# Performance work log

Hardware: AMD Instinct MI355X
Metric: run time of the kernel (lower is better)

The kernel has to match this reference:

```python
import jax, jax.numpy as jnp
import numpy as np

EMBED = 1024
HEADS = 16
HEAD_DIM = EMBED // HEADS
B, S = 4, 2048


def setup_inputs() -> dict:
    key = jax.random.key(0)
    ks = jax.random.split(key, 12)
    scale = 1.0 / np.sqrt(EMBED)
    inp = {
        'query': jax.random.normal(ks[0], (B, S, EMBED), jnp.float32),
        'key_in': jax.random.normal(ks[1], (B, S, EMBED), jnp.float32),
        'value': jax.random.normal(ks[2], (B, S, EMBED), jnp.float32),
        'mask': jnp.tril(jnp.ones((S, S), jnp.int32))[None, None],  # causal [1,1,S,S]
        'Wq': jax.random.normal(ks[3], (EMBED, EMBED), jnp.float32) * scale,
        'bq': jnp.zeros((EMBED,), jnp.float32),
        'Wk': jax.random.normal(ks[4], (EMBED, EMBED), jnp.float32) * scale,
        'bk': jnp.zeros((EMBED,), jnp.float32),
        'Wv': jax.random.normal(ks[5], (EMBED, EMBED), jnp.float32) * scale,
        'bv': jnp.zeros((EMBED,), jnp.float32),
        'Wo': jax.random.normal(ks[6], (EMBED, EMBED), jnp.float32) * scale,
        'bo': jnp.zeros((EMBED,), jnp.float32),
    }
    return inp


def reference(query, key_in, value, mask, Wq, bq, Wk, bk, Wv, bv, Wo, bo):
    b = query.shape[0]
    # projections (torch Linear: x @ W.T + b)
    Q = query @ Wq.T + bq
    K = key_in @ Wk.T + bk
    V = value @ Wv.T + bv
    # [B, H, S, Dh]
    Q = Q.reshape(b, -1, HEADS, HEAD_DIM).transpose(0, 2, 1, 3)
    K = K.reshape(b, -1, HEADS, HEAD_DIM).transpose(0, 2, 1, 3)
    V = V.reshape(b, -1, HEADS, HEAD_DIM).transpose(0, 2, 1, 3)
    scores = jnp.einsum('bhqd,bhkd->bhqk', Q, K) / np.sqrt(HEAD_DIM)
    scores = jnp.where(mask == 0, jnp.float32(-1e20), scores)
    probs = jax.nn.softmax(scores, axis=-1)  # dropout p=0 (eval)
    attn = jnp.einsum('bhqk,bhkd->bhqd', probs, V)
    attn = attn.transpose(0, 2, 1, 3).reshape(b, -1, EMBED)
    return attn @ Wo.T + bo
```

## Files before the change

kernel.cpp:

```cpp
#include <hip/hip_runtime.h>

typedef unsigned short u16;
typedef __bf16 bf16x8 __attribute__((ext_vector_type(8)));
typedef float f32x4 __attribute__((ext_vector_type(4)));

#define EMBED   1024
#define HEADS   16
#define HEAD_DIM 64
#define BATCH   4
#define SEQ     2048
#define MROWS   (BATCH * SEQ)

__device__ __forceinline__ u16 f2bf(float f) {
  union { __bf16 h; u16 u; } c;
  c.h = (__bf16)f;
  return c.u;
}

__device__ __forceinline__ bf16x8 cvt8(const float* p) {
  const float4 a = *(const float4*)p;
  const float4 b = *(const float4*)(p + 4);
  bf16x8 r;
  r[0] = (__bf16)a.x; r[1] = (__bf16)a.y; r[2] = (__bf16)a.z; r[3] = (__bf16)a.w;
  r[4] = (__bf16)b.x; r[5] = (__bf16)b.y; r[6] = (__bf16)b.z; r[7] = (__bf16)b.w;
  return r;
}

__device__ __forceinline__ void gload16(const u16* g, u16* lds) {
  __builtin_amdgcn_global_load_lds(
      (const __attribute__((address_space(1))) void*)g,
      (__attribute__((address_space(3))) void*)lds, 16, 0, 0);
}

__global__ __launch_bounds__(256) void cvt_bf16(
    const float* __restrict__ src, u16* __restrict__ dst, int n8)
{
  const int i = blockIdx.x * 256 + threadIdx.x;
  if (i < n8) *(bf16x8*)(dst + (size_t)i * 8) = cvt8(src + (size_t)i * 8);
}

__global__ __launch_bounds__(256) void cvt_a(
    const float* k,  u16* dk,  const float* v,  u16* dv,
    const float* wq, u16* dwq, const float* wk, u16* dwk,
    const float* wv, u16* dwv, int n8t, int n8w)
{
  int i = blockIdx.x * 256 + threadIdx.x;
  if (i < n8t) { *(bf16x8*)(dk + (size_t)i * 8) = cvt8(k + (size_t)i * 8); return; }
  i -= n8t;
  if (i < n8t) { *(bf16x8*)(dv + (size_t)i * 8) = cvt8(v + (size_t)i * 8); return; }
  i -= n8t;
  if (i < n8w) { *(bf16x8*)(dwq + (size_t)i * 8) = cvt8(wq + (size_t)i * 8); return; }
  i -= n8w;
  if (i < n8w) { *(bf16x8*)(dwk + (size_t)i * 8) = cvt8(wk + (size_t)i * 8); return; }
  i -= n8w;
  if (i < n8w) { *(bf16x8*)(dwv + (size_t)i * 8) = cvt8(wv + (size_t)i * 8); }
}

__device__ __forceinline__ void swz_block(int& m0, int& n0) {
  int bid = blockIdx.y * 8 + blockIdx.x;
  bid = (bid & 7) * 64 + (bid >> 3);
  m0 = (bid >> 3) * 128;
  n0 = (bid & 7) * 128;
}

#define GT_BK  64
#define GT_NT  (EMBED / GT_BK)
#define GT_BUF (128 * GT_BK * 2)

__global__ __launch_bounds__(256, 2) void gemm10(
    const u16* __restrict__ Aa, const u16* __restrict__ Ab,
    const u16* __restrict__ Wa, const u16* __restrict__ Wb,
    const float* __restrict__ biasa, const float* __restrict__ biasb,
    void* __restrict__ Ca, void* __restrict__ Cb, int fmode)
{
  __shared__ __align__(16) u16 smem[2 * GT_BUF];

  const int z = blockIdx.z;
  const u16* A      = z ? Ab : Aa;
  const u16* Bw     = z ? Wb : Wa;
  const float* bias = z ? biasb : biasa;
  void* C = z ? Cb : Ca;
  const int mode = z ? 1 : fmode;

  const int t    = threadIdx.x;
  const int lane = t & 63;
  const int wave = t >> 6;
  const int quad = lane >> 4;
  const int lr   = lane & 15;
  const int wr   = (wave >> 1) * 64;
  const int wc   = (wave & 1) * 64;
  int m0, n0;
  swz_block(m0, n0);

  const int sr = lane >> 3;
  const int sc = ((lane & 7) ^ sr) * 8;

  auto stage = [&](int b, int tt) {
    const int kb = tt * GT_BK;
    u16* s = smem + b * GT_BUF;
#pragma unroll
    for (int c8 = 0; c8 < 4; ++c8) {
      const int g = wave * 32 + c8 * 8;
      gload16(&A [(size_t)(m0 + g + sr) * EMBED + kb + sc], s + g * GT_BK);
      gload16(&Bw[(size_t)(n0 + g + sr) * EMBED + kb + sc], s + 128 * GT_BK + g * GT_BK);
    }
  };

  auto fragA = [&](int b, int mi, int ks) -> bf16x8 {
    const int row = wr + mi * 16 + lr;
    return *(const bf16x8*)(smem + b * GT_BUF + row * GT_BK
                            + (((ks * 4 + quad) ^ (row & 7)) << 3));
  };
  auto fragB = [&](int b, int ni, int ks) -> bf16x8 {
    const int row = wc + ni * 16 + lr;
    return *(const bf16x8*)(smem + b * GT_BUF + 128 * GT_BK + row * GT_BK
                            + (((ks * 4 + quad) ^ (row & 7)) << 3));
  };

  f32x4 acc[4][4] = {};

  stage(0, 0);
  asm volatile("s_waitcnt vmcnt(0)" ::: "memory");
  __builtin_amdgcn_s_barrier();
  __builtin_amdgcn_sched_barrier(0);

#pragma unroll 1
  for (int tt = 0; tt < GT_NT; ++tt) {
    const int cb = tt & 1;
    if (tt + 1 < GT_NT) stage(cb ^ 1, tt + 1);
#pragma unroll
    for (int ks = 0; ks < 2; ++ks) {
      bf16x8 af[4], bfr[4];
#pragma unroll
      for (int i = 0; i < 4; ++i) af[i]  = fragA(cb, i, ks);
#pragma unroll
      for (int i = 0; i < 4; ++i) bfr[i] = fragB(cb, i, ks);
      __builtin_amdgcn_s_setprio(1);
#pragma unroll
      for (int mi = 0; mi < 4; ++mi)
#pragma unroll
        for (int ni = 0; ni < 4; ++ni)
          acc[mi][ni] = __builtin_amdgcn_mfma_f32_16x16x32_bf16(af[mi], bfr[ni], acc[mi][ni], 0, 0, 0);
      __builtin_amdgcn_s_setprio(0);
    }
    asm volatile("s_waitcnt vmcnt(0)" ::: "memory");
    __builtin_amdgcn_s_barrier();
    __builtin_amdgcn_sched_barrier(0);
  }

  if (mode == 1) {
    u16* Vt = (u16*)C;
#pragma unroll
    for (int mi = 0; mi < 4; ++mi)
#pragma unroll
      for (int ni = 0; ni < 4; ++ni) {
        const int col = n0 + wc + ni * 16 + lr;
        const int hh = col >> 6, dd = col & 63;
        const float bv = bias[col];
        const int row0 = m0 + wr + mi * 16 + quad * 4;
        const int bb = row0 >> 11, s0 = row0 & 2047;
        u16 pk[4];
#pragma unroll
        for (int r = 0; r < 4; ++r) pk[r] = f2bf(acc[mi][ni][r] + bv);
        *(ushort4*)&Vt[((size_t)((bb * 16 + hh) * 64 + dd)) * SEQ + s0] = *(ushort4*)pk;
      }
  } else if (mode == 2) {
    float* Cf = (float*)C;
#pragma unroll
    for (int mi = 0; mi < 4; ++mi)
#pragma unroll
      for (int ni = 0; ni < 4; ++ni) {
        const int col = n0 + wc + ni * 16 + lr;
        const float bv = bias[col];
#pragma unroll
        for (int r = 0; r < 4; ++r) {
          const int row = m0 + wr + mi * 16 + quad * 4 + r;
          Cf[(size_t)row * EMBED + col] = acc[mi][ni][r] + bv;
        }
      }
  } else {
    u16* Cu = (u16*)C;
#pragma unroll
    for (int mi = 0; mi < 4; ++mi)
#pragma unroll
      for (int ni = 0; ni < 4; ++ni) {
        const int col = n0 + wc + ni * 16 + lr;
        const float bv = bias[col];
#pragma unroll
        for (int r = 0; r < 4; ++r) {
          const int row = m0 + wr + mi * 16 + quad * 4 + r;
          Cu[(size_t)row * EMBED + col] = f2bf(acc[mi][ni][r] + bv);
        }
      }
  }
}

#define F8_KV  (128 * 72)
#define F8_TILE (64 * 64)
__global__ __launch_bounds__(256, 3) void flash9(
    const u16* __restrict__ Qp, const u16* __restrict__ Kp,
    const u16* __restrict__ Vt, u16* __restrict__ AO)
{
  __shared__ __align__(16) u16 smem[F8_KV + 4 * F8_TILE];
  u16 (*Ps)[72] = (u16(*)[72])(smem);

  const int t    = threadIdx.x;
  const int lane = t & 63;
  const int wave = t >> 6;
  const int quad = lane >> 4;
  const int lr   = lane & 15;
  const int bh = blockIdx.x;
  const int qi = 15 - blockIdx.y;
  const int b  = bh >> 4, h = bh & 15;
  const size_t rowbase = (size_t)b * SEQ;
  const int hcol = h * HEAD_DIM;
  const int wrow = wave * 16;
  const int sr = lane >> 3;
  const int sc = ((lane & 7) ^ sr) * 8;

  auto frag = [&](int off, int row, int chunk) -> bf16x8 {
    return *(const bf16x8*)(smem + off + row * 64 + ((chunk ^ (row & 7)) << 3));
  };

  auto stageKV = [&](int bi, int j) {
    const int kb = j * 64;
    const int ko = F8_KV + bi * F8_TILE;
    const int vo = F8_KV + (2 + bi) * F8_TILE;
#pragma unroll
    for (int c8 = 0; c8 < 2; ++c8) {
      const int g = wrow + c8 * 8;
      gload16(&Kp[(rowbase + kb + g + sr) * EMBED + hcol + sc], smem + ko + g * 64);
      gload16(&Vt[((size_t)bh * 64 + g + sr) * SEQ + kb + sc],  smem + vo + g * 64);
    }
  };

  const int q0 = qi * 128;
  const int jmax = 2 * qi + 1;

  bf16x8 aq[2][2];
#pragma unroll
  for (int qg = 0; qg < 2; ++qg) {
    const u16* qrow = &Qp[(rowbase + q0 + qg * 64 + wrow + lr) * EMBED + hcol];
    aq[qg][0] = *(const bf16x8*)(qrow + quad * 8);
    aq[qg][1] = *(const bf16x8*)(qrow + 32 + quad * 8);
  }

  stageKV(0, 0);
  __syncthreads();

  f32x4 o0[4] = {}, o1[4] = {};
  float ls0 = 0.f, ls1 = 0.f;

  for (int j = 0; j <= jmax; ++j) {
    if (j < jmax) stageKV((j + 1) & 1, j + 1);
    const int ko = F8_KV + (j & 1) * F8_TILE;
    const int vo = F8_KV + (2 + (j & 1)) * F8_TILE;
    const bool a0 = (j <= 2 * qi);

    bf16x8 bk[2][4];
#pragma unroll
    for (int ks = 0; ks < 2; ++ks)
#pragma unroll
      for (int mi = 0; mi < 4; ++mi) bk[ks][mi] = frag(ko, mi * 16 + lr, ks * 4 + quad);

    if (a0) {
      f32x4 st[4] = {};
#pragma unroll
      for (int ks = 0; ks < 2; ++ks) {
        __builtin_amdgcn_s_setprio(1);
#pragma unroll
        for (int mi = 0; mi < 4; ++mi)
          st[mi] = __builtin_amdgcn_mfma_f32_16x16x32_bf16(bk[ks][mi], aq[0][ks], st[mi], 0, 0, 0);
        __builtin_amdgcn_s_setprio(0);
      }
      const bool diag = (j == 2 * qi);
#pragma unroll
      for (int mi = 0; mi < 4; ++mi) {
        union { ushort4 v; u16 e[4]; } pk;
#pragma unroll
        for (int r = 0; r < 4; ++r) {
          float p = __expf(st[mi][r] * 0.125f);
          if (diag && (mi * 16 + quad * 4 + r > wrow + lr)) p = 0.f;
          ls0 += p;
          pk.e[r] = f2bf(p);
        }
        *(ushort4*)&Ps[wrow + lr][mi * 16 + quad * 4] = pk.v;
      }
    }
    {
      f32x4 st[4] = {};
#pragma unroll
      for (int ks = 0; ks < 2; ++ks) {
        __builtin_amdgcn_s_setprio(1);
#pragma unroll
        for (int mi = 0; mi < 4; ++mi)
          st[mi] = __builtin_amdgcn_mfma_f32_16x16x32_bf16(bk[ks][mi], aq[1][ks], st[mi], 0, 0, 0);
        __builtin_amdgcn_s_setprio(0);
      }
      const bool diag = (j == jmax);
#pragma unroll
      for (int mi = 0; mi < 4; ++mi) {
        union { ushort4 v; u16 e[4]; } pk;
#pragma unroll
        for (int r = 0; r < 4; ++r) {
          float p = __expf(st[mi][r] * 0.125f);
          if (diag && (mi * 16 + quad * 4 + r > wrow + lr)) p = 0.f;
          ls1 += p;
          pk.e[r] = f2bf(p);
        }
        *(ushort4*)&Ps[64 + wrow + lr][mi * 16 + quad * 4] = pk.v;
      }
    }
#pragma unroll
    for (int ks = 0; ks < 2; ++ks) {
      bf16x8 bv[4];
#pragma unroll
      for (int nd = 0; nd < 4; ++nd) bv[nd] = frag(vo, nd * 16 + lr, ks * 4 + quad);
      const bf16x8 ap1 = *(const bf16x8*)&Ps[64 + wrow + lr][ks * 32 + quad * 8];
      __builtin_amdgcn_s_setprio(1);
      if (a0) {
        const bf16x8 ap0 = *(const bf16x8*)&Ps[wrow + lr][ks * 32 + quad * 8];
#pragma unroll
        for (int nd = 0; nd < 4; ++nd)
          o0[nd] = __builtin_amdgcn_mfma_f32_16x16x32_bf16(ap0, bv[nd], o0[nd], 0, 0, 0);
      }
#pragma unroll
      for (int nd = 0; nd < 4; ++nd)
        o1[nd] = __builtin_amdgcn_mfma_f32_16x16x32_bf16(ap1, bv[nd], o1[nd], 0, 0, 0);
      __builtin_amdgcn_s_setprio(0);
    }
    __syncthreads();
  }

#pragma unroll
  for (int qg = 0; qg < 2; ++qg) {
    float lsum = qg ? ls1 : ls0;
    lsum += __shfl_xor(lsum, 16);
    lsum += __shfl_xor(lsum, 32);
    float linv[4];
#pragma unroll
    for (int r = 0; r < 4; ++r)
      linv[r] = 1.0f / __shfl(lsum, quad * 4 + r);
    const f32x4* oo = qg ? o1 : o0;
#pragma unroll
    for (int nd = 0; nd < 4; ++nd)
#pragma unroll
      for (int r = 0; r < 4; ++r)
        AO[(rowbase + q0 + qg * 64 + wrow + quad * 4 + r) * EMBED + hcol + nd * 16 + lr]
            = f2bf(oo[nd][r] * linv[r]);
  }
}

extern "C" void kernel_launch(void* const* d_in, const int* in_sizes, int n_in,
                              void* d_out, int out_size, void* d_ws, size_t ws_size,
                              hipStream_t stream) {
  const float* query  = (const float*)d_in[0];
  const float* key_in = (const float*)d_in[1];
  const float* value  = (const float*)d_in[2];
  const float* Wq = (const float*)d_in[4];
  const float* bq = (const float*)d_in[5];
  const float* Wk = (const float*)d_in[6];
  const float* bk = (const float*)d_in[7];
  const float* Wv = (const float*)d_in[8];
  const float* bv = (const float*)d_in[9];
  const float* Wo = (const float*)d_in[10];
  const float* bo = (const float*)d_in[11];
  float* out = (float*)d_out;

  const size_t tsz = (size_t)MROWS * EMBED;
  const size_t wsz = (size_t)EMBED * EMBED;

  u16* Kp  = (u16*)d_ws;
  u16* Vt  = Kp + tsz;
  u16* Wob = Kp;

  u16* Kbf = (u16*)d_out;
  u16* Vbf = Kbf + tsz;
  u16* Qbf = Kbf;
  u16* Qp  = Vbf;

  u16* Wqb = (u16*)d_in[3];
  u16* Wkb = Wqb + wsz;
  u16* Wvb = Wkb + wsz;
  u16* AO  = (u16*)d_in[3];

  dim3 blk(256);
  const int n8t = (int)(tsz / 8), n8w = (int)(wsz / 8);

  cvt_a<<<(2 * n8t + 3 * n8w + 255) / 256, blk, 0, stream>>>(
      key_in, Kbf, value, Vbf, Wq, Wqb, Wk, Wkb, Wv, Wvb, n8t, n8w);

  gemm10<<<dim3(8, 64, 2), blk, 0, stream>>>(
      Kbf, Vbf, Wkb, Wvb, bk, bv, (void*)Kp, (void*)Vt, 0);

  cvt_bf16<<<n8t / 256, blk, 0, stream>>>(query, Qbf, n8t);

  gemm10<<<dim3(8, 64, 1), blk, 0, stream>>>(
      Qbf, nullptr, Wqb, nullptr, bq, nullptr, (void*)Qp, nullptr, 0);

  dim3 gattn(BATCH * HEADS, 16);
  flash9<<<gattn, blk, 0, stream>>>(Qp, Kp, Vt, AO);

  cvt_bf16<<<n8w / 256, blk, 0, stream>>>(Wo, Wob, n8w);

  gemm10<<<dim3(8, 64, 1), blk, 0, stream>>>(
      AO, nullptr, Wob, nullptr, bo, nullptr, (void*)out, nullptr, 2);
}
```

Baseline: 298.8 us.

## Fuse fp32-to-bf16 activation conversion into QKV GEMM and batch three projections

The Q, K and V projection GEMMs now read fp32 activations directly. Each tile is loaded into registers, converted to bf16 and written into the swizzled LDS layout, so the separate conversion kernels and their bf16 staging buffers are gone. All three projections also run in a single launch with blockIdx.z selecting the operand, which removes a launch and fills the device better. In exchange the GEMM reads twice the activation bytes per tile, and the A operand goes through registers instead of the async global-to-LDS path, which adds register pressure and a synchronous LDS write step each iteration.

```diff
diff --git a/kernel.cpp b/kernel.cpp
--- a/kernel.cpp
+++ b/kernel.cpp
@@ -1,4 +1,5 @@
 #include <hip/hip_runtime.h>
+#include <type_traits>
 
 typedef unsigned short u16;
 typedef __bf16 bf16x8 __attribute__((ext_vector_type(8)));
@@ -39,16 +40,11 @@
   if (i < n8) *(bf16x8*)(dst + (size_t)i * 8) = cvt8(src + (size_t)i * 8);
 }
 
-__global__ __launch_bounds__(256) void cvt_a(
-    const float* k,  u16* dk,  const float* v,  u16* dv,
+__global__ __launch_bounds__(256) void cvt_w3(
     const float* wq, u16* dwq, const float* wk, u16* dwk,
-    const float* wv, u16* dwv, int n8t, int n8w)
+    const float* wv, u16* dwv, int n8w)
 {
   int i = blockIdx.x * 256 + threadIdx.x;
-  if (i < n8t) { *(bf16x8*)(dk + (size_t)i * 8) = cvt8(k + (size_t)i * 8); return; }
-  i -= n8t;
-  if (i < n8t) { *(bf16x8*)(dv + (size_t)i * 8) = cvt8(v + (size_t)i * 8); return; }
-  i -= n8t;
   if (i < n8w) { *(bf16x8*)(dwq + (size_t)i * 8) = cvt8(wq + (size_t)i * 8); return; }
   i -= n8w;
   if (i < n8w) { *(bf16x8*)(dwk + (size_t)i * 8) = cvt8(wk + (size_t)i * 8); return; }
@@ -67,20 +63,21 @@
 #define GT_NT  (EMBED / GT_BK)
 #define GT_BUF (128 * GT_BK * 2)
 
-__global__ __launch_bounds__(256, 2) void gemm10(
-    const u16* __restrict__ Aa, const u16* __restrict__ Ab,
-    const u16* __restrict__ Wa, const u16* __restrict__ Wb,
-    const float* __restrict__ biasa, const float* __restrict__ biasb,
-    void* __restrict__ Ca, void* __restrict__ Cb, int fmode)
+template<typename TA>
+__global__ __launch_bounds__(256, 2) void gemm11(
+    const TA* __restrict__ A0, const TA* __restrict__ A1, const TA* __restrict__ A2,
+    const u16* __restrict__ W0, const u16* __restrict__ W1, const u16* __restrict__ W2,
+    const float* __restrict__ b0, const float* __restrict__ b1, const float* __restrict__ b2,
+    void* __restrict__ C0, void* __restrict__ C1, void* __restrict__ C2, int fmode)
 {
   __shared__ __align__(16) u16 smem[2 * GT_BUF];
 
   const int z = blockIdx.z;
-  const u16* A      = z ? Ab : Aa;
-  const u16* Bw     = z ? Wb : Wa;
-  const float* bias = z ? biasb : biasa;
-  void* C = z ? Cb : Ca;
-  const int mode = z ? 1 : fmode;
+  const TA* A       = (z == 0) ? A0 : (z == 1) ? A1 : A2;
+  const u16* Bw     = (z == 0) ? W0 : (z == 1) ? W1 : W2;
+  const float* bias = (z == 0) ? b0 : (z == 1) ? b1 : b2;
+  void* C           = (z == 0) ? C0 : (z == 1) ? C1 : C2;
+  const int mode = (z == 1) ? 1 : fmode;
 
   const int t    = threadIdx.x;
   const int lane = t & 63;
@@ -95,14 +92,48 @@
   const int sr = lane >> 3;
   const int sc = ((lane & 7) ^ sr) * 8;
 
-  auto stage = [&](int b, int tt) {
+  auto stageB = [&](int b, int tt) {
+    const int kb = tt * GT_BK;
+    u16* s = smem + b * GT_BUF + 128 * GT_BK;
+#pragma unroll
+    for (int c8 = 0; c8 < 4; ++c8) {
+      const int g = wave * 32 + c8 * 8;
+      gload16(&Bw[(size_t)(n0 + g + sr) * EMBED + kb + sc], s + g * GT_BK);
+    }
+  };
+
+  auto stageA_async = [&](int b, int tt) {
     const int kb = tt * GT_BK;
     u16* s = smem + b * GT_BUF;
 #pragma unroll
     for (int c8 = 0; c8 < 4; ++c8) {
       const int g = wave * 32 + c8 * 8;
-      gload16(&A [(size_t)(m0 + g + sr) * EMBED + kb + sc], s + g * GT_BK);
-      gload16(&Bw[(size_t)(n0 + g + sr) * EMBED + kb + sc], s + 128 * GT_BK + g * GT_BK);
+      gload16((const u16*)&A[(size_t)(m0 + g + sr) * EMBED + kb + sc], s + g * GT_BK);
+    }
+  };
+
+  float4 fr[4][2];
+  auto stageA_issue = [&](int tt) {
+    const int kb = tt * GT_BK;
+#pragma unroll
+    for (int c8 = 0; c8 < 4; ++c8) {
+      const int g = wave * 32 + c8 * 8;
+      const float* p = (const float*)&A[(size_t)(m0 + g + sr) * EMBED + kb + sc];
+      fr[c8][0] = *(const float4*)p;
+      fr[c8][1] = *(const float4*)(p + 4);
+    }
+  };
+  auto stageA_write = [&](int b) {
+    u16* s = smem + b * GT_BUF;
+#pragma unroll
+    for (int c8 = 0; c8 < 4; ++c8) {
+      const int g = wave * 32 + c8 * 8;
+      bf16x8 r;
+      r[0] = (__bf16)fr[c8][0].x; r[1] = (__bf16)fr[c8][0].y;
+      r[2] = (__bf16)fr[c8][0].z; r[3] = (__bf16)fr[c8][0].w;
+      r[4] = (__bf16)fr[c8][1].x; r[5] = (__bf16)fr[c8][1].y;
+      r[6] = (__bf16)fr[c8][1].z; r[7] = (__bf16)fr[c8][1].w;
+      *(bf16x8*)(s + (size_t)(g + sr) * GT_BK + (lane & 7) * 8) = r;
     }
   };
 
@@ -119,15 +150,29 @@
 
   f32x4 acc[4][4] = {};
 
-  stage(0, 0);
-  asm volatile("s_waitcnt vmcnt(0)" ::: "memory");
+  if constexpr (std::is_same<TA, float>::value) {
+    stageA_issue(0);
+    stageB(0, 0);
+    asm volatile("s_waitcnt vmcnt(0)" ::: "memory");
+    stageA_write(0);
+    asm volatile("s_waitcnt lgkmcnt(0)" ::: "memory");
+  } else {
+    stageA_async(0, 0);
+    stageB(0, 0);
+    asm volatile("s_waitcnt vmcnt(0)" ::: "memory");
+  }
   __builtin_amdgcn_s_barrier();
   __builtin_amdgcn_sched_barrier(0);
 
 #pragma unroll 1
   for (int tt = 0; tt < GT_NT; ++tt) {
     const int cb = tt & 1;
-    if (tt + 1 < GT_NT) stage(cb ^ 1, tt + 1);
+    const bool pf = (tt + 1 < GT_NT);
+    if (pf) {
+      if constexpr (std::is_same<TA, float>::value) stageA_issue(tt + 1);
+      else stageA_async(cb ^ 1, tt + 1);
+      stageB(cb ^ 1, tt + 1);
+    }
 #pragma unroll
     for (int ks = 0; ks < 2; ++ks) {
       bf16x8 af[4], bfr[4];
@@ -144,6 +189,10 @@
       __builtin_amdgcn_s_setprio(0);
     }
     asm volatile("s_waitcnt vmcnt(0)" ::: "memory");
+    if constexpr (std::is_same<TA, float>::value) {
+      if (pf) stageA_write(cb ^ 1);
+      asm volatile("s_waitcnt lgkmcnt(0)" ::: "memory");
+    }
     __builtin_amdgcn_s_barrier();
     __builtin_amdgcn_sched_barrier(0);
   }
@@ -374,10 +423,7 @@
   u16* Vt  = Kp + tsz;
   u16* Wob = Kp;
 
-  u16* Kbf = (u16*)d_out;
-  u16* Vbf = Kbf + tsz;
-  u16* Qbf = Kbf;
-  u16* Qp  = Vbf;
+  u16* Qp = (u16*)d_out;
 
   u16* Wqb = (u16*)d_in[3];
   u16* Wkb = Wqb + wsz;
@@ -385,24 +431,21 @@
   u16* AO  = (u16*)d_in[3];
 
   dim3 blk(256);
-  const int n8t = (int)(tsz / 8), n8w = (int)(wsz / 8);
-
-  cvt_a<<<(2 * n8t + 3 * n8w + 255) / 256, blk, 0, stream>>>(
-      key_in, Kbf, value, Vbf, Wq, Wqb, Wk, Wkb, Wv, Wvb, n8t, n8w);
-
-  gemm10<<<dim3(8, 64, 2), blk, 0, stream>>>(
-      Kbf, Vbf, Wkb, Wvb, bk, bv, (void*)Kp, (void*)Vt, 0);
-
-  cvt_bf16<<<n8t / 256, blk, 0, stream>>>(query, Qbf, n8t);
-
-  gemm10<<<dim3(8, 64, 1), blk, 0, stream>>>(
-      Qbf, nullptr, Wqb, nullptr, bq, nullptr, (void*)Qp, nullptr, 0);
+  const int n8w = (int)(wsz / 8);
+
+  cvt_w3<<<(3 * n8w + 255) / 256, blk, 0, stream>>>(
+      Wq, Wqb, Wk, Wkb, Wv, Wvb, n8w);
+
+  gemm11<float><<<dim3(8, 64, 3), blk, 0, stream>>>(
+      key_in, value, query, Wkb, Wvb, Wqb, bk, bv, bq,
+      (void*)Kp, (void*)Vt, (void*)Qp, 0);
 
   dim3 gattn(BATCH * HEADS, 16);
   flash9<<<gattn, blk, 0, stream>>>(Qp, Kp, Vt, AO);
 
   cvt_bf16<<<n8w / 256, blk, 0, stream>>>(Wo, Wob, n8w);
 
-  gemm10<<<dim3(8, 64, 1), blk, 0, stream>>>(
-      AO, nullptr, Wob, nullptr, bo, nullptr, (void*)out, nullptr, 2);
-}
+  gemm11<u16><<<dim3(8, 64, 1), blk, 0, stream>>>(
+      AO, nullptr, nullptr, Wob, nullptr, nullptr, bo, nullptr, nullptr,
+      (void*)out, nullptr, nullptr, 2);
+}
```

After: 317.5 us. 1.06x slower.
